# Performance work log

Hardware: AMD Instinct MI355X
Metric: run time of the kernel (lower is better)

Reference implementation:

```python
import jax, jax.numpy as jnp
import numpy as np

EPS = 1e-5
GROUPS = 32


def group_norm(x, w, b):
    # x: [N, C]; GroupNorm over 1x1 spatial == per-group norm over C//GROUPS chans
    N, C = x.shape
    xg = x.reshape(N, GROUPS, C // GROUPS)
    mu = xg.mean(-1, keepdims=True)
    var = xg.var(-1, keepdims=True)
    xn = ((xg - mu) * jax.lax.rsqrt(var + EPS)).reshape(N, C)
    return xn * w + b


def rb(x, gn1w, gn1b, c1w, c1b, gn2w, gn2b, c2w, c2b):
    # Conv2d 3x3 pad=1 on a 1x1 spatial input: only the center tap sees data
    # (all other taps hit zero padding), so it reduces exactly to a GEMM with
    # the [out, in] center slice of the kernel.
    h = jax.nn.silu(group_norm(x, gn1w, gn1b))
    h = h @ c1w[:, :, 1, 1].T + c1b
    h = jax.nn.silu(group_norm(h, gn2w, gn2b))
    h = h @ c2w[:, :, 1, 1].T + c2b
    return h + x  # skip == Identity (in_ch == out_ch)


def setup_inputs() -> dict:
    key = jax.random.key(0)
    ks = jax.random.split(key, 20)
    BS, CAND, D, H, W = 32, 2048, 256, 32, 32
    s = 0.05
    inp = {
        "gimage": jax.random.normal(ks[0], (BS, D, H, W), dtype=jnp.float32),
        "pts": jax.random.randint(ks[1], (BS, CAND, 1, 2), 0, 256, dtype=jnp.int32),
        # two stacked RB blocks
        "gn1_w": jnp.ones((2, D), jnp.float32),
        "gn1_b": jnp.zeros((2, D), jnp.float32),
        "conv1_w": jax.random.normal(ks[2], (2, D, D, 3, 3), jnp.float32) * s,
        "conv1_b": jnp.zeros((2, D), jnp.float32),
        "gn2_w": jnp.ones((2, D), jnp.float32),
        "gn2_b": jnp.zeros((2, D), jnp.float32),
        "conv2_w": jax.random.normal(ks[3], (2, D, D, 3, 3), jnp.float32) * s,
        "conv2_b": jnp.zeros((2, D), jnp.float32),
        # class_embed: Linear(256, 2)
        "cls_w": jax.random.normal(ks[4], (2, D), jnp.float32) * s,
        "cls_b": jnp.zeros((2,), jnp.float32),
        # bbox_embed: MLP(256, 256, 4, 3)
        "mlp_w1": jax.random.normal(ks[5], (D, D), jnp.float32) * s,
        "mlp_b1": jnp.zeros((D,), jnp.float32),
        "mlp_w2": jax.random.normal(ks[6], (D, D), jnp.float32) * s,
        "mlp_b2": jnp.zeros((D,), jnp.float32),
        "mlp_w3": jax.random.normal(ks[7], (4, D), jnp.float32) * s,
        "mlp_b3": jnp.zeros((4,), jnp.float32),
    }
    return inp


def reference(gimage, pts, gn1_w, gn1_b, conv1_w, conv1_b, gn2_w, gn2_b,
              conv2_w, conv2_b, cls_w, cls_b, mlp_w1, mlp_b1, mlp_w2, mlp_b2,
              mlp_w3, mlp_b3):
    bs, C, H, W = gimage.shape
    c = pts.shape[1]
    # patch_idx = (pts // 8)[:, :, 0, :] -> (iy, ix) per (batch, candidate)
    idx = pts[:, :, 0, :] // 8                      # [bs, c, 2]
    lin = idx[..., 0] * W + idx[..., 1]             # [bs, c] flat spatial index
    g = gimage.reshape(bs, C, H * W)
    feat = jnp.take_along_axis(g, lin[:, None, :].astype(jnp.int32), axis=2)  # [bs, C, c]
    x = feat.transpose(0, 2, 1).reshape(bs * c, C)  # [(bs c), 256]

    for i in range(2):  # convLayer = Sequential(RB, RB)
        x = rb(x, gn1_w[i], gn1_b[i], conv1_w[i], conv1_b[i],
               gn2_w[i], gn2_b[i], conv2_w[i], conv2_b[i])

    logits = x @ cls_w.T + cls_b                    # [(bs c), 2]
    h = jax.nn.relu(x @ mlp_w1.T + mlp_b1)
    h = jax.nn.relu(h @ mlp_w2.T + mlp_b2)
    boxes = jax.nn.sigmoid(h @ mlp_w3.T + mlp_b3)   # [(bs c), 4]

    pred_logits = logits.reshape(bs, c, 2)
    pred_boxes = boxes.reshape(bs, c, 4)
    return pred_logits, pred_boxes
```

## Files before the change

kernel.cpp:

```cpp
#include <hip/hip_runtime.h>


typedef __attribute__((ext_vector_type(8))) _Float16 half8;
typedef __attribute__((ext_vector_type(4))) float f32x4;

#define AS 264

#define NHALF  393216
#define OFF_WC1 0
#define OFF_WC2 131072
#define OFF_W1  262144
#define OFF_W2  327680
#define WS_NEED 1572864

__device__ __forceinline__ float sigm(float y) { return 1.f / (1.f + __expf(-y)); }

__global__ __launch_bounds__(256) void prep(const float* __restrict__ c1w,
                                            const float* __restrict__ c2w,
                                            const float* __restrict__ w1,
                                            const float* __restrict__ w2,
                                            _Float16* __restrict__ ws) {
  int i = blockIdx.x * 256 + threadIdx.x;
  {
    float v = c1w[(size_t)i * 9 + 4];
    _Float16 h = (_Float16)v;
    ws[OFF_WC1 + i] = h;
    ws[NHALF + OFF_WC1 + i] = (_Float16)(v - (float)h);
  }
  {
    float v = c2w[(size_t)i * 9 + 4];
    _Float16 h = (_Float16)v;
    ws[OFF_WC2 + i] = h;
    ws[NHALF + OFF_WC2 + i] = (_Float16)(v - (float)h);
  }
  if (i < 65536) {
    float v = w1[i];
    _Float16 h = (_Float16)v;
    ws[OFF_W1 + i] = h;
    ws[NHALF + OFF_W1 + i] = (_Float16)(v - (float)h);
    v = w2[i];
    h = (_Float16)v;
    ws[OFF_W2 + i] = h;
    ws[NHALF + OFF_W2 + i] = (_Float16)(v - (float)h);
  }
}

__device__ __forceinline__ void hl_store(_Float16* __restrict__ Ah,
                                         _Float16* __restrict__ Al,
                                         int idx, float v) {
  _Float16 h = (_Float16)v;
  Ah[idx] = h;
  Al[idx] = (_Float16)(v - (float)h);
}

__device__ __forceinline__ void mfma_run(f32x4 acc[2][4],
    const _Float16* __restrict__ Ah, const _Float16* __restrict__ Al,
    const _Float16* __restrict__ Wh, const _Float16* __restrict__ Wl,
    int aoff, size_t boff) {
  half8 bh[4], bl[4];
  #pragma unroll
  for (int nt = 0; nt < 4; nt++) {
    bh[nt] = *(const half8*)(Wh + boff + (nt << 12));
    bl[nt] = *(const half8*)(Wl + boff + (nt << 12));
  }
  #pragma unroll
  for (int mt = 0; mt < 2; mt++)
    #pragma unroll
    for (int nt = 0; nt < 4; nt++)
      acc[mt][nt] = (f32x4){0.f, 0.f, 0.f, 0.f};
  __syncthreads();
  #pragma unroll
  for (int kt = 0; kt < 8; kt++) {
    half8 ah0 = *(const half8*)(Ah + aoff + kt * 32);
    half8 ah1 = *(const half8*)(Ah + aoff + 16 * AS + kt * 32);
    half8 al0 = *(const half8*)(Al + aoff + kt * 32);
    half8 al1 = *(const half8*)(Al + aoff + 16 * AS + kt * 32);
    #pragma unroll
    for (int nt = 0; nt < 4; nt++) {
      acc[0][nt] = __builtin_amdgcn_mfma_f32_16x16x32_f16(ah0, bh[nt], acc[0][nt], 0, 0, 0);
      acc[1][nt] = __builtin_amdgcn_mfma_f32_16x16x32_f16(ah1, bh[nt], acc[1][nt], 0, 0, 0);
      acc[0][nt] = __builtin_amdgcn_mfma_f32_16x16x32_f16(ah0, bl[nt], acc[0][nt], 0, 0, 0);
      acc[1][nt] = __builtin_amdgcn_mfma_f32_16x16x32_f16(ah1, bl[nt], acc[1][nt], 0, 0, 0);
      acc[0][nt] = __builtin_amdgcn_mfma_f32_16x16x32_f16(al0, bh[nt], acc[0][nt], 0, 0, 0);
      acc[1][nt] = __builtin_amdgcn_mfma_f32_16x16x32_f16(al1, bh[nt], acc[1][nt], 0, 0, 0);
    }
    if (kt < 7) {
      #pragma unroll
      for (int nt = 0; nt < 4; nt++) {
        bh[nt] = *(const half8*)(Wh + boff + (nt << 12) + (kt + 1) * 32);
        bl[nt] = *(const half8*)(Wl + boff + (nt << 12) + (kt + 1) * 32);
      }
    }
  }
}

__device__ __forceinline__ void gn_x_to_A(const float x[2][4][4],
    const float* __restrict__ gnw, const float* __restrict__ gnb,
    int col, int quad, int nb,
    _Float16* __restrict__ Ah, _Float16* __restrict__ Al) {
  #pragma unroll
  for (int nt = 0; nt < 4; nt++) {
    int n = nb + (nt << 4) + col;
    float gwv = gnw[n], gbv = gnb[n];
    #pragma unroll
    for (int mt = 0; mt < 2; mt++) {
      #pragma unroll
      for (int rg = 0; rg < 4; rg++) {
        float v = x[mt][nt][rg];
        float s = v, q = v * v;
        s += __shfl_xor(s, 1); q += __shfl_xor(q, 1);
        s += __shfl_xor(s, 2); q += __shfl_xor(q, 2);
        s += __shfl_xor(s, 4); q += __shfl_xor(q, 4);
        float mu = s * 0.125f;
        float rs = rsqrtf(q * 0.125f - mu * mu + 1e-5f);
        float y = (v - mu) * rs * gwv + gbv;
        float sv = y * sigm(y);
        hl_store(Ah, Al, ((mt << 4) + (quad << 2) + rg) * AS + n, sv);
      }
    }
  }
}

__device__ __forceinline__ void epi_gn_to_A(const f32x4 acc[2][4],
    const float* __restrict__ bias,
    const float* __restrict__ gnw, const float* __restrict__ gnb,
    int col, int quad, int nb,
    _Float16* __restrict__ Ah, _Float16* __restrict__ Al) {
  #pragma unroll
  for (int nt = 0; nt < 4; nt++) {
    int n = nb + (nt << 4) + col;
    float bv = bias[n];
    float gwv = gnw[n], gbv = gnb[n];
    #pragma unroll
    for (int mt = 0; mt < 2; mt++) {
      #pragma unroll
      for (int rg = 0; rg < 4; rg++) {
        float v = acc[mt][nt][rg] + bv;
        float s = v, q = v * v;
        s += __shfl_xor(s, 1); q += __shfl_xor(q, 1);
        s += __shfl_xor(s, 2); q += __shfl_xor(q, 2);
        s += __shfl_xor(s, 4); q += __shfl_xor(q, 4);
        float mu = s * 0.125f;
        float rs = rsqrtf(q * 0.125f - mu * mu + 1e-5f);
        float y = (v - mu) * rs * gwv + gbv;
        float sv = y * sigm(y);
        hl_store(Ah, Al, ((mt << 4) + (quad << 2) + rg) * AS + n, sv);
      }
    }
  }
}

__device__ __forceinline__ void epi_relu_to_A(const f32x4 acc[2][4],
    const float* __restrict__ bias, int col, int quad, int nb,
    _Float16* __restrict__ Ah, _Float16* __restrict__ Al) {
  #pragma unroll
  for (int nt = 0; nt < 4; nt++) {
    int n = nb + (nt << 4) + col;
    float bv = bias[n];
    #pragma unroll
    for (int mt = 0; mt < 2; mt++)
      #pragma unroll
      for (int rg = 0; rg < 4; rg++)
        hl_store(Ah, Al, ((mt << 4) + (quad << 2) + rg) * AS + n,
                 fmaxf(acc[mt][nt][rg] + bv, 0.f));
  }
}

__global__ __launch_bounds__(256, 3) void fused_mfma(
    const float* __restrict__ gimage, const int* __restrict__ pts,
    const float* __restrict__ gn1w, const float* __restrict__ gn1b,
    const float* __restrict__ c1b,
    const float* __restrict__ gn2w, const float* __restrict__ gn2b,
    const float* __restrict__ c2b,
    const float* __restrict__ clsw, const float* __restrict__ clsb,
    const float* __restrict__ b1, const float* __restrict__ b2,
    const float* __restrict__ w3, const float* __restrict__ b3,
    const _Float16* __restrict__ ws, float* __restrict__ out) {
  __shared__ _Float16 Ah[32 * AS];
  __shared__ _Float16 Al[32 * AS];
  __shared__ float red[4][32][4];

  const int t = threadIdx.x;
  const int w = t >> 6;
  const int lane = t & 63;
  const int col = lane & 15;
  const int quad = lane >> 4;
  const int nb = w << 6;
  const int bsw = ((blockIdx.x & 7) << 8) | (blockIdx.x >> 3);
  const int row0 = bsw << 5;
  const int rbase = quad << 2;

  const int aoff = col * AS + (quad << 3);
  const size_t boff = (((size_t)(nb + col)) << 8) + (quad << 3);
  const _Float16* wsl = ws + NHALF;

  float x[2][4][4];
  {
    int lin[2][4];
    #pragma unroll
    for (int mt = 0; mt < 2; mt++)
      #pragma unroll
      for (int rg = 0; rg < 4; rg++) {
        int grow = row0 + (mt << 4) + rbase + rg;
        int p0 = pts[2 * grow], p1 = pts[2 * grow + 1];
        lin[mt][rg] = ((p0 >> 3) << 5) + (p1 >> 3);
      }
    const float* gbase = gimage + (((size_t)((row0 >> 11) << 8)) << 10);
    #pragma unroll
    for (int nt = 0; nt < 4; nt++) {
      const float* gc = gbase + (((size_t)(nb + (nt << 4) + col)) << 10);
      #pragma unroll
      for (int mt = 0; mt < 2; mt++)
        #pragma unroll
        for (int rg = 0; rg < 4; rg++)
          x[mt][nt][rg] = gc[lin[mt][rg]];
    }
  }

  f32x4 acc[2][4];

  #pragma unroll 1
  for (int rb = 0; rb < 2; rb++) {
    gn_x_to_A(x, gn1w + (rb << 8), gn1b + (rb << 8), col, quad, nb, Ah, Al);
    mfma_run(acc, Ah, Al, ws + OFF_WC1 + (rb << 16), wsl + OFF_WC1 + (rb << 16),
             aoff, boff);
    __syncthreads();
    epi_gn_to_A(acc, c1b + (rb << 8), gn2w + (rb << 8), gn2b + (rb << 8),
                col, quad, nb, Ah, Al);
    mfma_run(acc, Ah, Al, ws + OFF_WC2 + (rb << 16), wsl + OFF_WC2 + (rb << 16),
             aoff, boff);
    __syncthreads();
    #pragma unroll
    for (int nt = 0; nt < 4; nt++) {
      float bv = c2b[(rb << 8) + nb + (nt << 4) + col];
      #pragma unroll
      for (int mt = 0; mt < 2; mt++)
        #pragma unroll
        for (int rg = 0; rg < 4; rg++)
          x[mt][nt][rg] += acc[mt][nt][rg] + bv;
    }
  }

  #pragma unroll
  for (int nt = 0; nt < 4; nt++) {
    int n = nb + (nt << 4) + col;
    #pragma unroll
    for (int mt = 0; mt < 2; mt++)
      #pragma unroll
      for (int rg = 0; rg < 4; rg++)
        hl_store(Ah, Al, ((mt << 4) + rbase + rg) * AS + n, x[mt][nt][rg]);
  }
  {
    float pc[2][2][4];
    #pragma unroll
    for (int j = 0; j < 2; j++) {
      #pragma unroll
      for (int mt = 0; mt < 2; mt++)
        #pragma unroll
        for (int rg = 0; rg < 4; rg++)
          pc[j][mt][rg] = 0.f;
      #pragma unroll
      for (int nt = 0; nt < 4; nt++) {
        float wv = clsw[(j << 8) + nb + (nt << 4) + col];
        #pragma unroll
        for (int mt = 0; mt < 2; mt++)
          #pragma unroll
          for (int rg = 0; rg < 4; rg++)
            pc[j][mt][rg] += x[mt][nt][rg] * wv;
      }
    }
    #pragma unroll
    for (int j = 0; j < 2; j++)
      #pragma unroll
      for (int mt = 0; mt < 2; mt++)
        #pragma unroll
        for (int rg = 0; rg < 4; rg++) {
          float p = pc[j][mt][rg];
          p += __shfl_xor(p, 1);
          p += __shfl_xor(p, 2);
          p += __shfl_xor(p, 4);
          p += __shfl_xor(p, 8);
          if (col == 0) red[w][(mt << 4) + rbase + rg][j] = p;
        }
  }

  mfma_run(acc, Ah, Al, ws + OFF_W1, wsl + OFF_W1, aoff, boff);
  if (t < 64) {
    int r = t >> 1, j = t & 1;
    out[((size_t)(row0 + r) << 1) + j] =
        clsb[j] + red[0][r][j] + red[1][r][j] + red[2][r][j] + red[3][r][j];
  }
  __syncthreads();
  epi_relu_to_A(acc, b1, col, quad, nb, Ah, Al);

  mfma_run(acc, Ah, Al, ws + OFF_W2, wsl + OFF_W2, aoff, boff);
  __syncthreads();
  {
    float pb[4][2][4];
    #pragma unroll
    for (int j = 0; j < 4; j++)
      #pragma unroll
      for (int mt = 0; mt < 2; mt++)
        #pragma unroll
        for (int rg = 0; rg < 4; rg++)
          pb[j][mt][rg] = 0.f;
    #pragma unroll
    for (int nt = 0; nt < 4; nt++) {
      int n = nb + (nt << 4) + col;
      float bv = b2[n];
      float w0 = w3[n], w1v = w3[256 + n], w2v = w3[512 + n], w3v = w3[768 + n];
      #pragma unroll
      for (int mt = 0; mt < 2; mt++)
        #pragma unroll
        for (int rg = 0; rg < 4; rg++) {
          float v = fmaxf(acc[mt][nt][rg] + bv, 0.f);
          pb[0][mt][rg] += v * w0;
          pb[1][mt][rg] += v * w1v;
          pb[2][mt][rg] += v * w2v;
          pb[3][mt][rg] += v * w3v;
        }
    }
    #pragma unroll
    for (int j = 0; j < 4; j++)
      #pragma unroll
      for (int mt = 0; mt < 2; mt++)
        #pragma unroll
        for (int rg = 0; rg < 4; rg++) {
          float p = pb[j][mt][rg];
          p += __shfl_xor(p, 1);
          p += __shfl_xor(p, 2);
          p += __shfl_xor(p, 4);
          p += __shfl_xor(p, 8);
          if (col == 0) red[w][(mt << 4) + rbase + rg][j] = p;
        }
  }
  __syncthreads();
  if (t < 128) {
    int r = t >> 2, j = t & 3;
    float s = b3[j] + red[0][r][j] + red[1][r][j] + red[2][r][j] + red[3][r][j];
    out[131072 + ((size_t)(row0 + r) << 2) + j] = sigm(s);
  }
}

#define LS 260
template <int EPI, bool CONV>
__device__ __forceinline__ void gemm_f32(const float* __restrict__ src,
                                         const float* __restrict__ W,
                                         const float* __restrict__ bias,
                                         float* __restrict__ dst,
                                         float* __restrict__ X) {
  const int n = threadIdx.x;
  float acc[32];
  #pragma unroll
  for (int r = 0; r < 32; r++) acc[r] = 0.f;
  #pragma unroll 1
  for (int k = 0; k < 256; k += 8) {
    float w[8];
    if (CONV) {
      #pragma unroll
      for (int j = 0; j < 8; j++) w[j] = W[(size_t)((n << 8) + k + j) * 9 + 4];
    } else {
      f32x4 wa = *(const f32x4*)(W + (n << 8) + k);
      f32x4 wb = *(const f32x4*)(W + (n << 8) + k + 4);
      w[0] = wa[0]; w[1] = wa[1]; w[2] = wa[2]; w[3] = wa[3];
      w[4] = wb[0]; w[5] = wb[1]; w[6] = wb[2]; w[7] = wb[3];
    }
    #pragma unroll
    for (int r = 0; r < 32; r++) {
      const float* xr = src + r * LS + k;
      f32x4 a0 = *(const f32x4*)xr, a1 = *(const f32x4*)(xr + 4);
      acc[r] += a0[0] * w[0] + a0[1] * w[1] + a0[2] * w[2] + a0[3] * w[3]
              + a1[0] * w[4] + a1[1] * w[5] + a1[2] * w[6] + a1[7 - 7] * w[7] * 0.f
              + a1[3] * w[7];
    }
  }
  float bv = bias[n];
  #pragma unroll
  for (int r = 0; r < 32; r++) {
    float v = acc[r] + bv;
    if (EPI == 0) dst[r * LS + n] = v;
    else if (EPI == 1) X[r * LS + n] += v;
    else dst[r * LS + n] = fmaxf(v, 0.f);
  }
}
__device__ __forceinline__ void gn_silu32(const float* __restrict__ src,
                                          float* __restrict__ dst,
                                          const float* __restrict__ gw,
                                          const float* __restrict__ gb, int t) {
  #pragma unroll
  for (int i = 0; i < 4; i++) {
    int task = (i << 8) + t;
    int r = task >> 5, g = task & 31;
    const float* x = src + r * LS + (g << 3);
    f32x4 x0 = *(const f32x4*)x, x1 = *(const f32x4*)(x + 4);
    float xx[8] = {x0[0], x0[1], x0[2], x0[3], x1[0], x1[1], x1[2], x1[3]};
    float s = 0.f, q = 0.f;
    #pragma unroll
    for (int j = 0; j < 8; j++) { s += xx[j]; q += xx[j] * xx[j]; }
    float mu = s * 0.125f;
    float rs = rsqrtf(q * 0.125f - mu * mu + 1e-5f);
    const float* w = gw + (g << 3);
    const float* b = gb + (g << 3);
    float* d = dst + r * LS + (g << 3);
    #pragma unroll
    for (int j = 0; j < 8; j++) {
      float y = (xx[j] - mu) * rs * w[j] + b[j];
      d[j] = y * sigm(y);
    }
  }
}
__global__ __launch_bounds__(256, 1) void fused_all(
    const float* __restrict__ gimage, const int* __restrict__ pts,
    const float* __restrict__ gn1w, const float* __restrict__ gn1b,
    const float* __restrict__ c1w, const float* __restrict__ c1b,
    const float* __restrict__ gn2w, const float* __restrict__ gn2b,
    const float* __restrict__ c2w, const float* __restrict__ c2b,
    const float* __restrict__ clsw, const float* __restrict__ clsb,
    const float* __restrict__ w1, const float* __restrict__ b1,
    const float* __restrict__ w2, const float* __restrict__ b2,
    const float* __restrict__ w3, const float* __restrict__ b3,
    float* __restrict__ out) {
  __shared__ float X[32 * LS];
  __shared__ float A[32 * LS];
  __shared__ float H[32 * LS];
  const int t = threadIdx.x;
  const int row0 = blockIdx.x << 5;
  {
    int r = t >> 3;
    int c0 = (t & 7) << 5;
    int grow = row0 + r;
    int p0 = pts[2 * grow], p1 = pts[2 * grow + 1];
    int lin = ((p0 >> 3) << 5) + (p1 >> 3);
    int b = grow >> 11;
    const float* src = gimage + (((size_t)((b << 8) + c0)) << 10) + lin;
    #pragma unroll
    for (int c = 0; c < 32; c++) X[r * LS + c0 + c] = src[(size_t)c << 10];
  }
  __syncthreads();
  #pragma unroll 1
  for (int rb = 0; rb < 2; rb++) {
    gn_silu32(X, A, gn1w + (rb << 8), gn1b + (rb << 8), t);
    __syncthreads();
    gemm_f32<0, true>(A, c1w + rb * 589824, c1b + (rb << 8), H, nullptr);
    __syncthreads();
    gn_silu32(H, A, gn2w + (rb << 8), gn2b + (rb << 8), t);
    __syncthreads();
    gemm_f32<1, true>(A, c2w + rb * 589824, c2b + (rb << 8), nullptr, X);
    __syncthreads();
  }
  if (t < 64) {
    int r = t >> 1, j = t & 1;
    float s = clsb[j];
    const float* w = clsw + (j << 8);
    const float* x = X + r * LS;
    #pragma unroll 1
    for (int k = 0; k < 256; k += 4) {
      f32x4 wv = *(const f32x4*)(w + k);
      f32x4 xv = *(const f32x4*)(x + k);
      s += xv[0] * wv[0] + xv[1] * wv[1] + xv[2] * wv[2] + xv[3] * wv[3];
    }
    out[((size_t)(row0 + r) << 1) + j] = s;
  }
  gemm_f32<2, false>(X, w1, b1, H, nullptr);
  __syncthreads();
  gemm_f32<2, false>(H, w2, b2, A, nullptr);
  __syncthreads();
  if (t < 128) {
    int r = t >> 2, j = t & 3;
    float s = b3[j];
    const float* w = w3 + (j << 8);
    const float* x = A + r * LS;
    #pragma unroll 1
    for (int k = 0; k < 256; k += 4) {
      f32x4 wv = *(const f32x4*)(w + k);
      f32x4 xv = *(const f32x4*)(x + k);
      s += xv[0] * wv[0] + xv[1] * wv[1] + xv[2] * wv[2] + xv[3] * wv[3];
    }
    out[131072 + ((size_t)(row0 + r) << 2) + j] = sigm(s);
  }
}

extern "C" void kernel_launch(void* const* d_in, const int* in_sizes, int n_in,
                              void* d_out, int out_size, void* d_ws, size_t ws_size,
                              hipStream_t stream) {
  const float* gimage = (const float*)d_in[0];
  const int* pts = (const int*)d_in[1];
  const float* gn1w = (const float*)d_in[2];
  const float* gn1b = (const float*)d_in[3];
  const float* c1w = (const float*)d_in[4];
  const float* c1b = (const float*)d_in[5];
  const float* gn2w = (const float*)d_in[6];
  const float* gn2b = (const float*)d_in[7];
  const float* c2w = (const float*)d_in[8];
  const float* c2b = (const float*)d_in[9];
  const float* clsw = (const float*)d_in[10];
  const float* clsb = (const float*)d_in[11];
  const float* w1 = (const float*)d_in[12];
  const float* b1 = (const float*)d_in[13];
  const float* w2 = (const float*)d_in[14];
  const float* b2 = (const float*)d_in[15];
  const float* w3 = (const float*)d_in[16];
  const float* b3 = (const float*)d_in[17];

  if (ws_size >= (size_t)WS_NEED) {
    _Float16* ws = (_Float16*)d_ws;
    prep<<<512, 256, 0, stream>>>(c1w, c2w, w1, w2, ws);
    fused_mfma<<<2048, 256, 0, stream>>>(gimage, pts, gn1w, gn1b, c1b,
                                         gn2w, gn2b, c2b, clsw, clsb,
                                         b1, b2, w3, b3, ws, (float*)d_out);
  } else {
    fused_all<<<2048, 256, 0, stream>>>(gimage, pts, gn1w, gn1b, c1w, c1b,
                                        gn2w, gn2b, c2w, c2b, clsw, clsb,
                                        w1, b1, w2, b2, w3, b3, (float*)d_out);
  }
}
```

Baseline: 534.3 us.

## Prefetch next GEMM weights across epilogues and use DPP for group reductions

Splits the MFMA routine so the first k-slice of the next layer's weight fragments is loaded into registers before the current epilogue runs. This hides global or L2 latency behind the GroupNorm/SiLU work. Group-of-8 and group-of-16 sums now use DPP row operations instead of ds_swizzle/shuffle-based __shfl_xor, which cuts cross-lane instruction latency. Also removes a dead multiply-by-zero term in the fp32 fallback GEMM. The prefetch keeps extra B registers live through the epilogues, which raises register pressure and may reduce occupancy.

```diff
diff --git a/kernel.cpp b/kernel.cpp
--- a/kernel.cpp
+++ b/kernel.cpp
@@ -14,6 +14,32 @@
 #define WS_NEED 1572864
 
 __device__ __forceinline__ float sigm(float y) { return 1.f / (1.f + __expf(-y)); }
+
+template <int CTRL>
+__device__ __forceinline__ float dppadd(float v) {
+  union { float f; int i; } u, r;
+  u.f = v;
+  r.i = __builtin_amdgcn_update_dpp(0, u.i, CTRL, 0xf, 0xf, true);
+  return v + r.f;
+}
+#define DPP_X1 0xB1
+#define DPP_X2 0x4E
+#define DPP_X7 0x141
+#define DPP_XF 0x140
+
+__device__ __forceinline__ float gsum8(float v) {
+  v = dppadd<DPP_X1>(v);
+  v = dppadd<DPP_X2>(v);
+  v = dppadd<DPP_X7>(v);
+  return v;
+}
+__device__ __forceinline__ float gsum16(float v) {
+  v = dppadd<DPP_X1>(v);
+  v = dppadd<DPP_X2>(v);
+  v = dppadd<DPP_X7>(v);
+  v = dppadd<DPP_XF>(v);
+  return v;
+}
 
 __global__ __launch_bounds__(256) void prep(const float* __restrict__ c1w,
                                             const float* __restrict__ c2w,
@@ -53,16 +79,22 @@
   Al[idx] = (_Float16)(v - (float)h);
 }
 
-__device__ __forceinline__ void mfma_run(f32x4 acc[2][4],
+struct BF { half8 h[4], l[4]; };
+
+__device__ __forceinline__ void preloadB(BF& B,
+    const _Float16* __restrict__ Wh, const _Float16* __restrict__ Wl,
+    size_t boff) {
+  #pragma unroll
+  for (int nt = 0; nt < 4; nt++) {
+    B.h[nt] = *(const half8*)(Wh + boff + (nt << 12));
+    B.l[nt] = *(const half8*)(Wl + boff + (nt << 12));
+  }
+}
+
+__device__ __forceinline__ void mfma_body(f32x4 acc[2][4], BF& B,
     const _Float16* __restrict__ Ah, const _Float16* __restrict__ Al,
     const _Float16* __restrict__ Wh, const _Float16* __restrict__ Wl,
     int aoff, size_t boff) {
-  half8 bh[4], bl[4];
-  #pragma unroll
-  for (int nt = 0; nt < 4; nt++) {
-    bh[nt] = *(const half8*)(Wh + boff + (nt << 12));
-    bl[nt] = *(const half8*)(Wl + boff + (nt << 12));
-  }
   #pragma unroll
   for (int mt = 0; mt < 2; mt++)
     #pragma unroll
@@ -77,18 +109,18 @@
     half8 al1 = *(const half8*)(Al + aoff + 16 * AS + kt * 32);
     #pragma unroll
     for (int nt = 0; nt < 4; nt++) {
-      acc[0][nt] = __builtin_amdgcn_mfma_f32_16x16x32_f16(ah0, bh[nt], acc[0][nt], 0, 0, 0);
-      acc[1][nt] = __builtin_amdgcn_mfma_f32_16x16x32_f16(ah1, bh[nt], acc[1][nt], 0, 0, 0);
-      acc[0][nt] = __builtin_amdgcn_mfma_f32_16x16x32_f16(ah0, bl[nt], acc[0][nt], 0, 0, 0);
-      acc[1][nt] = __builtin_amdgcn_mfma_f32_16x16x32_f16(ah1, bl[nt], acc[1][nt], 0, 0, 0);
-      acc[0][nt] = __builtin_amdgcn_mfma_f32_16x16x32_f16(al0, bh[nt], acc[0][nt], 0, 0, 0);
-      acc[1][nt] = __builtin_amdgcn_mfma_f32_16x16x32_f16(al1, bh[nt], acc[1][nt], 0, 0, 0);
+      acc[0][nt] = __builtin_amdgcn_mfma_f32_16x16x32_f16(ah0, B.h[nt], acc[0][nt], 0, 0, 0);
+      acc[1][nt] = __builtin_amdgcn_mfma_f32_16x16x32_f16(ah1, B.h[nt], acc[1][nt], 0, 0, 0);
+      acc[0][nt] = __builtin_amdgcn_mfma_f32_16x16x32_f16(ah0, B.l[nt], acc[0][nt], 0, 0, 0);
+      acc[1][nt] = __builtin_amdgcn_mfma_f32_16x16x32_f16(ah1, B.l[nt], acc[1][nt], 0, 0, 0);
+      acc[0][nt] = __builtin_amdgcn_mfma_f32_16x16x32_f16(al0, B.h[nt], acc[0][nt], 0, 0, 0);
+      acc[1][nt] = __builtin_amdgcn_mfma_f32_16x16x32_f16(al1, B.h[nt], acc[1][nt], 0, 0, 0);
     }
     if (kt < 7) {
       #pragma unroll
       for (int nt = 0; nt < 4; nt++) {
-        bh[nt] = *(const half8*)(Wh + boff + (nt << 12) + (kt + 1) * 32);
-        bl[nt] = *(const half8*)(Wl + boff + (nt << 12) + (kt + 1) * 32);
+        B.h[nt] = *(const half8*)(Wh + boff + (nt << 12) + (kt + 1) * 32);
+        B.l[nt] = *(const half8*)(Wl + boff + (nt << 12) + (kt + 1) * 32);
       }
     }
   }
@@ -107,10 +139,8 @@
       #pragma unroll
       for (int rg = 0; rg < 4; rg++) {
         float v = x[mt][nt][rg];
-        float s = v, q = v * v;
-        s += __shfl_xor(s, 1); q += __shfl_xor(q, 1);
-        s += __shfl_xor(s, 2); q += __shfl_xor(q, 2);
-        s += __shfl_xor(s, 4); q += __shfl_xor(q, 4);
+        float s = gsum8(v);
+        float q = gsum8(v * v);
         float mu = s * 0.125f;
         float rs = rsqrtf(q * 0.125f - mu * mu + 1e-5f);
         float y = (v - mu) * rs * gwv + gbv;
@@ -136,10 +166,8 @@
       #pragma unroll
       for (int rg = 0; rg < 4; rg++) {
         float v = acc[mt][nt][rg] + bv;
-        float s = v, q = v * v;
-        s += __shfl_xor(s, 1); q += __shfl_xor(q, 1);
-        s += __shfl_xor(s, 2); q += __shfl_xor(q, 2);
-        s += __shfl_xor(s, 4); q += __shfl_xor(q, 4);
+        float s = gsum8(v);
+        float q = gsum8(v * v);
         float mu = s * 0.125f;
         float rs = rsqrtf(q * 0.125f - mu * mu + 1e-5f);
         float y = (v - mu) * rs * gwv + gbv;
@@ -218,18 +246,25 @@
   }
 
   f32x4 acc[2][4];
-
+  BF B;
+
+  preloadB(B, ws + OFF_WC1, wsl + OFF_WC1, boff);
   #pragma unroll 1
   for (int rb = 0; rb < 2; rb++) {
     gn_x_to_A(x, gn1w + (rb << 8), gn1b + (rb << 8), col, quad, nb, Ah, Al);
-    mfma_run(acc, Ah, Al, ws + OFF_WC1 + (rb << 16), wsl + OFF_WC1 + (rb << 16),
-             aoff, boff);
+    mfma_body(acc, B, Ah, Al, ws + OFF_WC1 + (rb << 16),
+              wsl + OFF_WC1 + (rb << 16), aoff, boff);
     __syncthreads();
+    preloadB(B, ws + OFF_WC2 + (rb << 16), wsl + OFF_WC2 + (rb << 16), boff);
     epi_gn_to_A(acc, c1b + (rb << 8), gn2w + (rb << 8), gn2b + (rb << 8),
                 col, quad, nb, Ah, Al);
-    mfma_run(acc, Ah, Al, ws + OFF_WC2 + (rb << 16), wsl + OFF_WC2 + (rb << 16),
-             aoff, boff);
+    mfma_body(acc, B, Ah, Al, ws + OFF_WC2 + (rb << 16),
+              wsl + OFF_WC2 + (rb << 16), aoff, boff);
     __syncthreads();
+    if (rb == 0)
+      preloadB(B, ws + OFF_WC1 + 65536, wsl + OFF_WC1 + 65536, boff);
+    else
+      preloadB(B, ws + OFF_W1, wsl + OFF_W1, boff);
     #pragma unroll
     for (int nt = 0; nt < 4; nt++) {
       float bv = c2b[(rb << 8) + nb + (nt << 4) + col];
@@ -275,25 +310,22 @@
       for (int mt = 0; mt < 2; mt++)
         #pragma unroll
         for (int rg = 0; rg < 4; rg++) {
-          float p = pc[j][mt][rg];
-          p += __shfl_xor(p, 1);
-          p += __shfl_xor(p, 2);
-          p += __shfl_xor(p, 4);
-          p += __shfl_xor(p, 8);
+          float p = gsum16(pc[j][mt][rg]);
           if (col == 0) red[w][(mt << 4) + rbase + rg][j] = p;
         }
   }
 
-  mfma_run(acc, Ah, Al, ws + OFF_W1, wsl + OFF_W1, aoff, boff);
+  mfma_body(acc, B, Ah, Al, ws + OFF_W1, wsl + OFF_W1, aoff, boff);
   if (t < 64) {
     int r = t >> 1, j = t & 1;
     out[((size_t)(row0 + r) << 1) + j] =
         clsb[j] + red[0][r][j] + red[1][r][j] + red[2][r][j] + red[3][r][j];
   }
   __syncthreads();
+  preloadB(B, ws + OFF_W2, wsl + OFF_W2, boff);
   epi_relu_to_A(acc, b1, col, quad, nb, Ah, Al);
 
-  mfma_run(acc, Ah, Al, ws + OFF_W2, wsl + OFF_W2, aoff, boff);
+  mfma_body(acc, B, Ah, Al, ws + OFF_W2, wsl + OFF_W2, aoff, boff);
   __syncthreads();
   {
     float pb[4][2][4];
@@ -326,11 +358,7 @@
       for (int mt = 0; mt < 2; mt++)
         #pragma unroll
         for (int rg = 0; rg < 4; rg++) {
-          float p = pb[j][mt][rg];
-          p += __shfl_xor(p, 1);
-          p += __shfl_xor(p, 2);
-          p += __shfl_xor(p, 4);
-          p += __shfl_xor(p, 8);
+          float p = gsum16(pb[j][mt][rg]);
           if (col == 0) red[w][(mt << 4) + rbase + rg][j] = p;
         }
   }
@@ -370,8 +398,7 @@
       const float* xr = src + r * LS + k;
       f32x4 a0 = *(const f32x4*)xr, a1 = *(const f32x4*)(xr + 4);
       acc[r] += a0[0] * w[0] + a0[1] * w[1] + a0[2] * w[2] + a0[3] * w[3]
-              + a1[0] * w[4] + a1[1] * w[5] + a1[2] * w[6] + a1[7 - 7] * w[7] * 0.f
-              + a1[3] * w[7];
+              + a1[0] * w[4] + a1[1] * w[5] + a1[2] * w[6] + a1[3] * w[7];
     }
   }
   float bv = bias[n];
```

Result: faster. 494.8 us (-7.4%).
